# Kernel optimization log

Hardware: AMD Instinct MI355X
Metric: run time of the kernel (lower is better)

Reference implementation:

```python
import jax, jax.numpy as jnp
import numpy as np

N_HEADS = 16

def setup_inputs() -> dict:
    key = jax.random.key(0)
    ks = jax.random.split(key, 6)
    B, S, D = 2, 2048, 1024
    return {
        "hidden_states": jax.random.normal(ks[0], (B, S, D), dtype=jnp.float32),
        "Wq": jax.random.normal(ks[1], (D, D), dtype=jnp.float32) * (1.0 / np.sqrt(D)),
        "Wk": jax.random.normal(ks[2], (D, D), dtype=jnp.float32) * (1.0 / np.sqrt(D)),
        "Wv": jax.random.normal(ks[3], (D, D), dtype=jnp.float32) * (1.0 / np.sqrt(D)),
        "Wo": jax.random.normal(ks[4], (D, D), dtype=jnp.float32) * (1.0 / np.sqrt(D)),
        "bo": jnp.zeros((D,), dtype=jnp.float32),
    }

def reference(hidden_states, Wq, Wk, Wv, Wo, bo):
    B, S, D = hidden_states.shape
    H = N_HEADS
    hd = D // H  # head_dim; d_kv == d_model per module's final view
    # nn.Linear(bias=False): x @ W.T, then the module's direct view to (B, H, S, hd)
    q = (hidden_states @ Wq.T).reshape(B, H, S, hd)
    k = (hidden_states @ Wk.T).reshape(B, H, S, hd)  # self-attention path (encoder_states=None)
    v = (hidden_states @ Wv.T).reshape(B, H, S, hd)
    # naive full score matrix [B, H, S, S]
    wei = jnp.einsum('bhqd,bhkd->bhqk', q, k)
    causal = jnp.tril(jnp.ones((S, S), dtype=bool))
    wei = jnp.where(causal, wei, -jnp.inf)
    # NOTE: module divides logits by head_dim (not sqrt) -- preserved faithfully
    attn = jax.nn.softmax(wei / hd, axis=-1)
    ctx = jnp.einsum('bhqk,bhkd->bhqd', attn, v)  # [B, H, S, hd]
    out = ctx.transpose(0, 2, 1, 3).reshape(B, S, D)
    return out @ Wo.T + bo
```

## Files before the change

### kernel.cpp

```cpp
#include <hip/hip_runtime.h>

#define S_LEN   2048
#define D_MODEL 1024
#define N_HEADS 16
#define HEAD_DIM 64

typedef unsigned short u16;
typedef float  floatx4 __attribute__((ext_vector_type(4)));
typedef short  bf16x8  __attribute__((ext_vector_type(8)));
typedef short  bf16x4  __attribute__((ext_vector_type(4)));

__device__ __forceinline__ u16 f2bf(float f) {
    unsigned int u = __float_as_uint(f);
    u += 0x7FFF + ((u >> 16) & 1);
    return (u16)(u >> 16);
}
__device__ __forceinline__ unsigned pack2bf(float a, float b) {
    return (unsigned)f2bf(a) | ((unsigned)f2bf(b) << 16);
}

__device__ __forceinline__ void gload_lds16(const void* g, void* l) {
    __builtin_amdgcn_global_load_lds(
        reinterpret_cast<const __attribute__((address_space(1))) unsigned int*>(
            reinterpret_cast<uintptr_t>(g)),
        reinterpret_cast<__attribute__((address_space(3))) unsigned int*>(
            reinterpret_cast<uintptr_t>(l)),
        16, 0, 0);
}

__global__ __launch_bounds__(256) void cast_all(const float* __restrict__ hs,
                                                const float* __restrict__ w0,
                                                const float* __restrict__ w1,
                                                const float* __restrict__ w2,
                                                const float* __restrict__ w3,
                                                u16* __restrict__ dst) {
    const size_t NHS = (size_t)2 * S_LEN * D_MODEL;
    const size_t e0 = (size_t)blockIdx.x * 2048;
    const float* src;
    size_t base;
    if (e0 < NHS)                 { src = hs; base = 0; }
    else {
        const int wi = (int)((e0 - NHS) >> 20);
        src = wi == 0 ? w0 : wi == 1 ? w1 : wi == 2 ? w2 : w3;
        base = NHS + ((size_t)wi << 20);
    }
    const size_t i = e0 + (size_t)threadIdx.x * 8;
    const float4 a = *(const float4*)(src + (i - base));
    const float4 b = *(const float4*)(src + (i - base) + 4);
    uint4 o;
    o.x = pack2bf(a.x, a.y); o.y = pack2bf(a.z, a.w);
    o.z = pack2bf(b.x, b.y); o.w = pack2bf(b.z, b.w);
    *(uint4*)(dst + i) = o;
}

__global__ __launch_bounds__(256) void vtrans(const u16* __restrict__ Vf,
                                              u16* __restrict__ Vt) {
    __shared__ unsigned T[64 * 133];
    const int bh = blockIdx.y;
    const int sBase = blockIdx.x * 128;
    const u16* src = Vf + (size_t)bh * (S_LEN * HEAD_DIM) + (size_t)sBase * HEAD_DIM;
    u16* dst = Vt + (size_t)bh * (S_LEN * HEAD_DIM) + sBase;
    const int tid = threadIdx.x;

#pragma unroll
    for (int it = 0; it < 4; ++it) {
        const int idx = it * 256 + tid;
        const int row = idx >> 3, ch = idx & 7;
        const float4 v4 = *(const float4*)(src + row * 64 + ch * 8);
        const u16* vs = (const u16*)&v4;
#pragma unroll
        for (int j = 0; j < 8; ++j) T[(ch * 8 + j) * 133 + row] = vs[j];
    }
    __syncthreads();
#pragma unroll
    for (int it = 0; it < 4; ++it) {
        const int idx = it * 256 + tid;
        const int d = idx >> 4, sc = idx & 15;
        union { u16 u[8]; float4 f; } tmp;
#pragma unroll
        for (int j = 0; j < 8; ++j) tmp.u[j] = (u16)T[d * 133 + sc * 8 + j];
        *(float4*)(dst + (size_t)d * S_LEN + sc * 8) = tmp.f;
    }
}

__global__ __launch_bounds__(256, 3) void gemm_qkv(const u16* __restrict__ A,
                                                   const u16* __restrict__ Wq,
                                                   const u16* __restrict__ Wk,
                                                   const u16* __restrict__ Wv,
                                                   u16* __restrict__ Qo,
                                                   u16* __restrict__ Ko,
                                                   u16* __restrict__ Vfo) {
    __shared__ u16 As[128 * 64];
    __shared__ u16 Ws[128 * 64];

    const int blk = blockIdx.x;
    const int y   = (blk & 7) | (((blk >> 3) & 3) << 3);
    const int x   = blk >> 5;
    const int which = x >> 3;
    const int nBase = (x & 7) * 128;
    const int mBase = y * 128;
    const u16* W = which == 0 ? Wq : which == 1 ? Wk : Wv;

    const int tid = threadIdx.x, lane = tid & 63, wv = tid >> 6;
    const int l15 = lane & 15, quad = lane >> 4;
    const int wm = wv & 1, wn = wv >> 1;
    const int srow = lane >> 3;
    const int gch  = (lane & 7) ^ srow;
    const int swz  = l15 & 7;

    floatx4 acc[4][4];
#pragma unroll
    for (int i = 0; i < 4; ++i)
#pragma unroll
        for (int j = 0; j < 4; ++j) acc[i][j] = (floatx4)(0.0f);

    for (int k0 = 0; k0 < D_MODEL; k0 += 64) {
        __syncthreads();
#pragma unroll
        for (int t = 0; t < 4; ++t) {
            const int ci = wv * 4 + t;
            gload_lds16(A + (size_t)(mBase + ci * 8 + srow) * D_MODEL + k0 + gch * 8,
                        &As[ci * 512]);
            gload_lds16(W + (size_t)(nBase + ci * 8 + srow) * D_MODEL + k0 + gch * 8,
                        &Ws[ci * 512]);
        }
        __syncthreads();

#pragma unroll
        for (int ks = 0; ks < 2; ++ks) {
            bf16x8 af[4], bfr[4];
#pragma unroll
            for (int mt = 0; mt < 4; ++mt)
                af[mt] = *(const bf16x8*)&As[(wm * 64 + mt * 16 + l15) * 64
                                             + ((ks * 4 + quad) ^ swz) * 8];
#pragma unroll
            for (int nt = 0; nt < 4; ++nt)
                bfr[nt] = *(const bf16x8*)&Ws[(wn * 64 + nt * 16 + l15) * 64
                                              + ((ks * 4 + quad) ^ swz) * 8];
#pragma unroll
            for (int mt = 0; mt < 4; ++mt)
#pragma unroll
                for (int nt = 0; nt < 4; ++nt)
                    acc[mt][nt] = __builtin_amdgcn_mfma_f32_16x16x32_bf16(af[mt], bfr[nt], acc[mt][nt], 0, 0, 0);
        }
    }

    u16* O = which == 0 ? Qo : (which == 1 ? Ko : Vfo);
    const float scale = which == 0 ? (1.44269504088896f / 64.0f) : 1.0f;
#pragma unroll
    for (int mt = 0; mt < 4; ++mt)
#pragma unroll
        for (int nt = 0; nt < 4; ++nt) {
            const int col = nBase + wn * 64 + nt * 16 + l15;
#pragma unroll
            for (int r = 0; r < 4; ++r) {
                const int row = mBase + wm * 64 + mt * 16 + quad * 4 + r;
                O[(size_t)row * D_MODEL + col] = f2bf(acc[mt][nt][r] * scale);
            }
        }
}

__global__ __launch_bounds__(256, 3) void gemm_out(const u16* __restrict__ A,
                                                   const u16* __restrict__ W,
                                                   const float* __restrict__ bias,
                                                   float* __restrict__ C) {
    __shared__ u16 As[64 * 64];
    __shared__ u16 Ws[128 * 64];

    const int nBase = blockIdx.x * 128;
    const int mBase = blockIdx.y * 64;
    const int tid = threadIdx.x, lane = tid & 63, wv = tid >> 6;
    const int l15 = lane & 15, quad = lane >> 4;
    const int wm = wv & 1, wn = wv >> 1;
    const int srow = lane >> 3;
    const int gch  = (lane & 7) ^ srow;
    const int swz  = l15 & 7;

    floatx4 acc[2][4];
#pragma unroll
    for (int i = 0; i < 2; ++i)
#pragma unroll
        for (int j = 0; j < 4; ++j) acc[i][j] = (floatx4)(0.0f);

    for (int k0 = 0; k0 < D_MODEL; k0 += 64) {
        __syncthreads();
#pragma unroll
        for (int t = 0; t < 2; ++t) {
            const int ci = wv * 2 + t;
            gload_lds16(A + (size_t)(mBase + ci * 8 + srow) * D_MODEL + k0 + gch * 8,
                        &As[ci * 512]);
        }
#pragma unroll
        for (int t = 0; t < 4; ++t) {
            const int ci = wv * 4 + t;
            gload_lds16(W + (size_t)(nBase + ci * 8 + srow) * D_MODEL + k0 + gch * 8,
                        &Ws[ci * 512]);
        }
        __syncthreads();

#pragma unroll
        for (int ks = 0; ks < 2; ++ks) {
            bf16x8 af[2], bfr[4];
#pragma unroll
            for (int mt = 0; mt < 2; ++mt)
                af[mt] = *(const bf16x8*)&As[(wm * 32 + mt * 16 + l15) * 64
                                             + ((ks * 4 + quad) ^ swz) * 8];
#pragma unroll
            for (int nt = 0; nt < 4; ++nt)
                bfr[nt] = *(const bf16x8*)&Ws[(wn * 64 + nt * 16 + l15) * 64
                                              + ((ks * 4 + quad) ^ swz) * 8];
#pragma unroll
            for (int mt = 0; mt < 2; ++mt)
#pragma unroll
                for (int nt = 0; nt < 4; ++nt)
                    acc[mt][nt] = __builtin_amdgcn_mfma_f32_16x16x32_bf16(af[mt], bfr[nt], acc[mt][nt], 0, 0, 0);
        }
    }

#pragma unroll
    for (int mt = 0; mt < 2; ++mt)
#pragma unroll
        for (int nt = 0; nt < 4; ++nt) {
            const int col = nBase + wn * 64 + nt * 16 + l15;
            const float bv = bias[col];
#pragma unroll
            for (int r = 0; r < 4; ++r) {
                const int row = mBase + wm * 32 + mt * 16 + quad * 4 + r;
                C[(size_t)row * D_MODEL + col] = acc[mt][nt][r] + bv;
            }
        }
}

__global__ __launch_bounds__(256, 3) void attn6(const u16* __restrict__ Q,
                                                const u16* __restrict__ K,
                                                const u16* __restrict__ Vt,
                                                u16* __restrict__ Ctx) {
    __shared__ __align__(16) char smem[35840];
    u16*   Ks    = (u16*)smem;
    u16*   Vs    = (u16*)(smem + 16384);
    float* RedA  = (float*)smem;
    float* RedB  = (float*)(smem + 17408);
    float* lpbuf = (float*)(smem + 34816);

    const int flat = blockIdx.x;
    const int g    = flat & 31;
    const int qt   = 31 - (flat >> 5);
    const int h = g & 15, b = g >> 4;

    const int tid = threadIdx.x, lane = tid & 63, wv = tid >> 6;
    const int l15 = lane & 15, quad = lane >> 4;

    const size_t headOff = ((size_t)b * N_HEADS + h) * S_LEN * HEAD_DIM;
    const u16* Qh = Q + headOff;
    const u16* Kh = K + headOff;
    const u16* Vh = Vt + headOff;
    u16* Cb = Ctx + (size_t)b * S_LEN * D_MODEL + (size_t)h * HEAD_DIM;

    const int srow = lane >> 3;
    const int gch  = (lane & 7) ^ srow;
    const int swz  = l15 & 7;

    const int qBase = qt * 64;

    bf16x8 qb[4][2];
#pragma unroll
    for (int qg = 0; qg < 4; ++qg)
#pragma unroll
        for (int ks = 0; ks < 2; ++ks)
            qb[qg][ks] = *(const bf16x8*)(Qh + (size_t)(qBase + qg * 16 + l15) * 64
                                          + ks * 32 + quad * 8);

    floatx4 o[4][4];
#pragma unroll
    for (int qg = 0; qg < 4; ++qg)
#pragma unroll
        for (int dg = 0; dg < 4; ++dg) o[qg][dg] = (floatx4)(0.0f);
    float lp[4] = {0.0f, 0.0f, 0.0f, 0.0f};

#pragma unroll
    for (int t = 0; t < 2; ++t) {
        const int ci = wv * 2 + t;
        gload_lds16(Kh + (size_t)(ci * 8 + srow) * 64 + gch * 8, &Ks[ci * 512]);
        gload_lds16(Vh + (size_t)(ci * 8 + srow) * S_LEN + gch * 8, &Vs[ci * 512]);
    }
    __syncthreads();

    for (int kt = 0; kt <= qt; ++kt) {
        const int cur = (kt & 1) * 4096;
        const int nxt = 4096 - cur;

        if (kt < qt) {
            const int kB2 = (kt + 1) * 64;
#pragma unroll
            for (int t = 0; t < 2; ++t) {
                const int ci = wv * 2 + t;
                gload_lds16(Kh + (size_t)(kB2 + ci * 8 + srow) * 64 + gch * 8,
                            &Ks[nxt + ci * 512]);
                gload_lds16(Vh + (size_t)(ci * 8 + srow) * S_LEN + kB2 + gch * 8,
                            &Vs[nxt + ci * 512]);
            }
        }

        bf16x8 ka[2];
#pragma unroll
        for (int ks = 0; ks < 2; ++ks)
            ka[ks] = *(const bf16x8*)&Ks[cur + (wv * 16 + l15) * 64 + ((ks * 4 + quad) ^ swz) * 8];

        bf16x4 vb[4];
#pragma unroll
        for (int dg = 0; dg < 4; ++dg)
            vb[dg] = *(const bf16x4*)&Vs[cur + (dg * 16 + l15) * 64
                                         + (((wv * 2 + (quad >> 1)) ^ swz) * 8) + (quad & 1) * 4];

        floatx4 s[4];
#pragma unroll
        for (int qg = 0; qg < 4; ++qg) {
            s[qg] = (floatx4)(0.0f);
#pragma unroll
            for (int ks = 0; ks < 2; ++ks)
                s[qg] = __builtin_amdgcn_mfma_f32_16x16x32_bf16(ka[ks], qb[qg][ks], s[qg], 0, 0, 0);
        }

        const bool diag = (kt == qt);
#pragma unroll
        for (int qg = 0; qg < 4; ++qg) {
            if (diag && qg < wv) continue;
            float p[4];
#pragma unroll
            for (int r = 0; r < 4; ++r) {
                float pv = __builtin_amdgcn_exp2f(s[qg][r]);
                if (diag && qg == wv && (quad * 4 + r > l15)) pv = 0.0f;
                p[r] = pv;
                lp[qg] += pv;
            }
            union { uint2 u; bf16x4 v; } pk;
            pk.u.x = __builtin_amdgcn_perm(__float_as_uint(p[1]), __float_as_uint(p[0]), 0x07060302);
            pk.u.y = __builtin_amdgcn_perm(__float_as_uint(p[3]), __float_as_uint(p[2]), 0x07060302);
#pragma unroll
            for (int dg = 0; dg < 4; ++dg)
                o[qg][dg] = __builtin_amdgcn_mfma_f32_16x16x16bf16_1k(pk.v, vb[dg], o[qg][dg], 0, 0, 0);
        }

        __syncthreads();
    }

#pragma unroll
    for (int qg = 0; qg < 4; ++qg) {
        lp[qg] += __shfl_xor(lp[qg], 16);
        lp[qg] += __shfl_xor(lp[qg], 32);
    }
    lpbuf[wv * 64 + quad * 16 + l15] = lp[quad];

    if (wv == 1 || wv == 3) {
        float* R = (wv == 1) ? RedA : RedB;
#pragma unroll
        for (int qg = 0; qg < 4; ++qg)
#pragma unroll
            for (int dg = 0; dg < 4; ++dg)
                *(floatx4*)&R[(dg * 16 + l15) * 68 + qg * 16 + quad * 4] = o[qg][dg];
    }
    __syncthreads();
    if (wv == 0 || wv == 2) {
        const float* R = (wv == 0) ? RedA : RedB;
#pragma unroll
        for (int qg = 0; qg < 4; ++qg)
#pragma unroll
            for (int dg = 0; dg < 4; ++dg)
                o[qg][dg] += *(const floatx4*)&R[(dg * 16 + l15) * 68 + qg * 16 + quad * 4];
    }
    __syncthreads();
    if (wv == 2) {
#pragma unroll
        for (int qg = 0; qg < 4; ++qg)
#pragma unroll
            for (int dg = 0; dg < 4; ++dg)
                *(floatx4*)&RedA[(dg * 16 + l15) * 68 + qg * 16 + quad * 4] = o[qg][dg];
    }
    __syncthreads();
    if (wv == 0) {
#pragma unroll
        for (int qg = 0; qg < 4; ++qg) {
#pragma unroll
            for (int dg = 0; dg < 4; ++dg)
                o[qg][dg] += *(const floatx4*)&RedA[(dg * 16 + l15) * 68 + qg * 16 + quad * 4];
            floatx4 lt = *(const floatx4*)&lpbuf[0 * 64 + qg * 16 + quad * 4];
            lt += *(const floatx4*)&lpbuf[1 * 64 + qg * 16 + quad * 4];
            lt += *(const floatx4*)&lpbuf[2 * 64 + qg * 16 + quad * 4];
            lt += *(const floatx4*)&lpbuf[3 * 64 + qg * 16 + quad * 4];
#pragma unroll
            for (int r = 0; r < 4; ++r) {
                const float inv = 1.0f / lt[r];
                const int row = qBase + qg * 16 + quad * 4 + r;
#pragma unroll
                for (int dg = 0; dg < 4; ++dg)
                    Cb[(size_t)row * D_MODEL + dg * 16 + l15] = f2bf(o[qg][dg][r] * inv);
            }
        }
    }
}

extern "C" void kernel_launch(void* const* d_in, const int* in_sizes, int n_in,
                              void* d_out, int out_size, void* d_ws, size_t ws_size,
                              hipStream_t stream) {
    const float* hs = (const float*)d_in[0];
    const float* Wq = (const float*)d_in[1];
    const float* Wk = (const float*)d_in[2];
    const float* Wv = (const float*)d_in[3];
    const float* Wo = (const float*)d_in[4];
    const float* bo = (const float*)d_in[5];
    float* out = (float*)d_out;

    const size_t NHS = (size_t)2 * S_LEN * D_MODEL;
    const size_t NW  = (size_t)D_MODEL * D_MODEL;

    u16* hsb = (u16*)d_ws;
    u16* Wb  = hsb + NHS;
    u16* Qb  = Wb + 4 * NW;
    u16* Kb  = Qb + NHS;
    u16* Vfb = Kb + NHS;
    u16* Vtb = Vfb + NHS;
    u16* Cxb = Vtb + NHS;

    cast_all<<<4096, 256, 0, stream>>>(hs, Wq, Wk, Wv, Wo, hsb);

    gemm_qkv<<<768, 256, 0, stream>>>(hsb, Wb, Wb + NW, Wb + 2 * NW,
                                      Qb, Kb, Vfb);

    vtrans<<<dim3(16, 32), 256, 0, stream>>>(Vfb, Vtb);

    attn6<<<1024, 256, 0, stream>>>(Qb, Kb, Vtb, Cxb);

    gemm_out<<<dim3(8, 64), 256, 0, stream>>>(Cxb, Wb + 3 * NW, bo, out);
}
```

Measured before the change: 165.1 us.

## Drop V transpose kernel; read row-major V in attention with swapped MFMA operands

Removes the separate vtrans kernel and its extra global round trip. The attention kernel now loads V tiles in their natural row-major layout and gathers the B-operand with scalar u16 LDS reads. It swaps the PV MFMA operands so the output accumulators come out transposed, and reworks the cross-wave reduction and epilogue to match. It also raises wave priority around the MFMA section. The trade is one fewer launch and less memory traffic, against slower scalar LDS gathers in the inner loop and an extra reduction barrier.

```diff
diff --git a/kernel.cpp b/kernel.cpp
--- a/kernel.cpp
+++ b/kernel.cpp
@@ -53,36 +53,6 @@
     *(uint4*)(dst + i) = o;
 }
 
-__global__ __launch_bounds__(256) void vtrans(const u16* __restrict__ Vf,
-                                              u16* __restrict__ Vt) {
-    __shared__ unsigned T[64 * 133];
-    const int bh = blockIdx.y;
-    const int sBase = blockIdx.x * 128;
-    const u16* src = Vf + (size_t)bh * (S_LEN * HEAD_DIM) + (size_t)sBase * HEAD_DIM;
-    u16* dst = Vt + (size_t)bh * (S_LEN * HEAD_DIM) + sBase;
-    const int tid = threadIdx.x;
-
-#pragma unroll
-    for (int it = 0; it < 4; ++it) {
-        const int idx = it * 256 + tid;
-        const int row = idx >> 3, ch = idx & 7;
-        const float4 v4 = *(const float4*)(src + row * 64 + ch * 8);
-        const u16* vs = (const u16*)&v4;
-#pragma unroll
-        for (int j = 0; j < 8; ++j) T[(ch * 8 + j) * 133 + row] = vs[j];
-    }
-    __syncthreads();
-#pragma unroll
-    for (int it = 0; it < 4; ++it) {
-        const int idx = it * 256 + tid;
-        const int d = idx >> 4, sc = idx & 15;
-        union { u16 u[8]; float4 f; } tmp;
-#pragma unroll
-        for (int j = 0; j < 8; ++j) tmp.u[j] = (u16)T[d * 133 + sc * 8 + j];
-        *(float4*)(dst + (size_t)d * S_LEN + sc * 8) = tmp.f;
-    }
-}
-
 __global__ __launch_bounds__(256, 3) void gemm_qkv(const u16* __restrict__ A,
                                                    const u16* __restrict__ Wq,
                                                    const u16* __restrict__ Wk,
@@ -233,7 +203,7 @@
 
 __global__ __launch_bounds__(256, 3) void attn6(const u16* __restrict__ Q,
                                                 const u16* __restrict__ K,
-                                                const u16* __restrict__ Vt,
+                                                const u16* __restrict__ Vf,
                                                 u16* __restrict__ Ctx) {
     __shared__ __align__(16) char smem[35840];
     u16*   Ks    = (u16*)smem;
@@ -253,7 +223,7 @@
     const size_t headOff = ((size_t)b * N_HEADS + h) * S_LEN * HEAD_DIM;
     const u16* Qh = Q + headOff;
     const u16* Kh = K + headOff;
-    const u16* Vh = Vt + headOff;
+    const u16* Vh = Vf + headOff;
     u16* Cb = Ctx + (size_t)b * S_LEN * D_MODEL + (size_t)h * HEAD_DIM;
 
     const int srow = lane >> 3;
@@ -281,7 +251,7 @@
     for (int t = 0; t < 2; ++t) {
         const int ci = wv * 2 + t;
         gload_lds16(Kh + (size_t)(ci * 8 + srow) * 64 + gch * 8, &Ks[ci * 512]);
-        gload_lds16(Vh + (size_t)(ci * 8 + srow) * S_LEN + gch * 8, &Vs[ci * 512]);
+        gload_lds16(Vh + (size_t)(ci * 8 + srow) * 64 + gch * 8, &Vs[ci * 512]);
     }
     __syncthreads();
 
@@ -296,7 +266,7 @@
                 const int ci = wv * 2 + t;
                 gload_lds16(Kh + (size_t)(kB2 + ci * 8 + srow) * 64 + gch * 8,
                             &Ks[nxt + ci * 512]);
-                gload_lds16(Vh + (size_t)(ci * 8 + srow) * S_LEN + kB2 + gch * 8,
+                gload_lds16(Vh + (size_t)(kB2 + ci * 8 + srow) * 64 + gch * 8,
                             &Vs[nxt + ci * 512]);
             }
         }
@@ -308,10 +278,21 @@
 
         bf16x4 vb[4];
 #pragma unroll
-        for (int dg = 0; dg < 4; ++dg)
-            vb[dg] = *(const bf16x4*)&Vs[cur + (dg * 16 + l15) * 64
-                                         + (((wv * 2 + (quad >> 1)) ^ swz) * 8) + (quad & 1) * 4];
-
+        for (int dg = 0; dg < 4; ++dg) {
+            u16 tmp[4];
+#pragma unroll
+            for (int j = 0; j < 4; ++j) {
+                const int R = wv * 16 + quad * 4 + j;
+                const int d = dg * 16 + l15;
+                const int slot = (d >> 3) ^ (R & 7);
+                tmp[j] = Vs[cur + R * 64 + slot * 8 + (d & 7)];
+            }
+            bf16x4 v; v[0] = (short)tmp[0]; v[1] = (short)tmp[1];
+            v[2] = (short)tmp[2]; v[3] = (short)tmp[3];
+            vb[dg] = v;
+        }
+
+        __builtin_amdgcn_s_setprio(1);
         floatx4 s[4];
 #pragma unroll
         for (int qg = 0; qg < 4; ++qg) {
@@ -338,8 +319,9 @@
             pk.u.y = __builtin_amdgcn_perm(__float_as_uint(p[3]), __float_as_uint(p[2]), 0x07060302);
 #pragma unroll
             for (int dg = 0; dg < 4; ++dg)
-                o[qg][dg] = __builtin_amdgcn_mfma_f32_16x16x16bf16_1k(pk.v, vb[dg], o[qg][dg], 0, 0, 0);
-        }
+                o[qg][dg] = __builtin_amdgcn_mfma_f32_16x16x16bf16_1k(vb[dg], pk.v, o[qg][dg], 0, 0, 0);
+        }
+        __builtin_amdgcn_s_setprio(0);
 
         __syncthreads();
     }
@@ -357,7 +339,9 @@
         for (int qg = 0; qg < 4; ++qg)
 #pragma unroll
             for (int dg = 0; dg < 4; ++dg)
-                *(floatx4*)&R[(dg * 16 + l15) * 68 + qg * 16 + quad * 4] = o[qg][dg];
+#pragma unroll
+                for (int r = 0; r < 4; ++r)
+                    R[(dg * 16 + quad * 4 + r) * 68 + qg * 16 + l15] = o[qg][dg][r];
     }
     __syncthreads();
     if (wv == 0 || wv == 2) {
@@ -366,7 +350,9 @@
         for (int qg = 0; qg < 4; ++qg)
 #pragma unroll
             for (int dg = 0; dg < 4; ++dg)
-                o[qg][dg] += *(const floatx4*)&R[(dg * 16 + l15) * 68 + qg * 16 + quad * 4];
+#pragma unroll
+                for (int r = 0; r < 4; ++r)
+                    o[qg][dg][r] += R[(dg * 16 + quad * 4 + r) * 68 + qg * 16 + l15];
     }
     __syncthreads();
     if (wv == 2) {
@@ -374,15 +360,27 @@
         for (int qg = 0; qg < 4; ++qg)
 #pragma unroll
             for (int dg = 0; dg < 4; ++dg)
-                *(floatx4*)&RedA[(dg * 16 + l15) * 68 + qg * 16 + quad * 4] = o[qg][dg];
+#pragma unroll
+                for (int r = 0; r < 4; ++r)
+                    RedA[(dg * 16 + quad * 4 + r) * 68 + qg * 16 + l15] = o[qg][dg][r];
     }
     __syncthreads();
     if (wv == 0) {
 #pragma unroll
+        for (int qg = 0; qg < 4; ++qg)
+#pragma unroll
+            for (int dg = 0; dg < 4; ++dg)
+#pragma unroll
+                for (int r = 0; r < 4; ++r) {
+                    const float v = o[qg][dg][r]
+                        + RedA[(dg * 16 + quad * 4 + r) * 68 + qg * 16 + l15];
+                    RedB[(dg * 16 + quad * 4 + r) * 68 + qg * 16 + l15] = v;
+                }
+    }
+    __syncthreads();
+    if (wv == 0) {
+#pragma unroll
         for (int qg = 0; qg < 4; ++qg) {
-#pragma unroll
-            for (int dg = 0; dg < 4; ++dg)
-                o[qg][dg] += *(const floatx4*)&RedA[(dg * 16 + l15) * 68 + qg * 16 + quad * 4];
             floatx4 lt = *(const floatx4*)&lpbuf[0 * 64 + qg * 16 + quad * 4];
             lt += *(const floatx4*)&lpbuf[1 * 64 + qg * 16 + quad * 4];
             lt += *(const floatx4*)&lpbuf[2 * 64 + qg * 16 + quad * 4];
@@ -392,8 +390,10 @@
                 const float inv = 1.0f / lt[r];
                 const int row = qBase + qg * 16 + quad * 4 + r;
 #pragma unroll
-                for (int dg = 0; dg < 4; ++dg)
-                    Cb[(size_t)row * D_MODEL + dg * 16 + l15] = f2bf(o[qg][dg][r] * inv);
+                for (int dg = 0; dg < 4; ++dg) {
+                    const float v = RedB[(dg * 16 + l15) * 68 + qg * 16 + quad * 4 + r];
+                    Cb[(size_t)row * D_MODEL + dg * 16 + l15] = f2bf(v * inv);
+                }
             }
         }
     }
@@ -418,17 +418,14 @@
     u16* Qb  = Wb + 4 * NW;
     u16* Kb  = Qb + NHS;
     u16* Vfb = Kb + NHS;
-    u16* Vtb = Vfb + NHS;
-    u16* Cxb = Vtb + NHS;
+    u16* Cxb = Vfb + NHS;
 
     cast_all<<<4096, 256, 0, stream>>>(hs, Wq, Wk, Wv, Wo, hsb);
 
     gemm_qkv<<<768, 256, 0, stream>>>(hsb, Wb, Wb + NW, Wb + 2 * NW,
                                       Qb, Kb, Vfb);
 
-    vtrans<<<dim3(16, 32), 256, 0, stream>>>(Vfb, Vtb);
-
-    attn6<<<1024, 256, 0, stream>>>(Qb, Kb, Vtb, Cxb);
+    attn6<<<1024, 256, 0, stream>>>(Qb, Kb, Vfb, Cxb);
 
     gemm_out<<<dim3(8, 64), 256, 0, stream>>>(Cxb, Wb + 3 * NW, bo, out);
 }
```

Result: no change. 166.9 us (+1.1%).

## Merge two adjacent query tiles per 512-thread attention block sharing K/V tiles

Applied to the files above, without the earlier changes.

The attention kernel now runs 8 waves per block, with two 64-row query tiles (paired as 2qp and 2qp+1) sharing each staged K/V tile. This halves global-to-LDS K/V traffic per query row and halves the block count. The block order is also changed so heavy and light causal pairs interleave for better load balance. The cost is more LDS per block (about 70 KB) and idle waves on the lower tile's final key step. It also needs a larger reduction scratch area.

```diff
diff --git a/kernel.cpp b/kernel.cpp
--- a/kernel.cpp
+++ b/kernel.cpp
@@ -231,24 +231,27 @@
         }
 }
 
-__global__ __launch_bounds__(256, 3) void attn6(const u16* __restrict__ Q,
+__global__ __launch_bounds__(512, 4) void attn8(const u16* __restrict__ Q,
                                                 const u16* __restrict__ K,
                                                 const u16* __restrict__ Vt,
                                                 u16* __restrict__ Ctx) {
-    __shared__ __align__(16) char smem[35840];
+    __shared__ __align__(16) char smem[71680];
     u16*   Ks    = (u16*)smem;
     u16*   Vs    = (u16*)(smem + 16384);
-    float* RedA  = (float*)smem;
-    float* RedB  = (float*)(smem + 17408);
-    float* lpbuf = (float*)(smem + 34816);
+    float* lpbuf = (float*)(smem + 69632);
 
     const int flat = blockIdx.x;
     const int g    = flat & 31;
-    const int qt   = 31 - (flat >> 5);
+    const int jj   = flat >> 5;
+    const int qp   = (jj < 8) ? (15 - jj) : (jj - 8);
     const int h = g & 15, b = g >> 4;
 
     const int tid = threadIdx.x, lane = tid & 63, wv = tid >> 6;
+    const int kw = wv & 3, qh = wv >> 2;
     const int l15 = lane & 15, quad = lane >> 4;
+
+    float* R0 = (float*)(smem + qh * 34816);
+    float* R1 = (float*)(smem + qh * 34816 + 17408);
 
     const size_t headOff = ((size_t)b * N_HEADS + h) * S_LEN * HEAD_DIM;
     const u16* Qh = Q + headOff;
@@ -260,7 +263,9 @@
     const int gch  = (lane & 7) ^ srow;
     const int swz  = l15 & 7;
 
-    const int qBase = qt * 64;
+    const int qBase = (qp * 2 + qh) * 64;
+    const int qtw   = qp * 2 + qh;
+    const int qtmax = qp * 2 + 1;
 
     bf16x8 qb[4][2];
 #pragma unroll
@@ -277,68 +282,63 @@
         for (int dg = 0; dg < 4; ++dg) o[qg][dg] = (floatx4)(0.0f);
     float lp[4] = {0.0f, 0.0f, 0.0f, 0.0f};
 
-#pragma unroll
-    for (int t = 0; t < 2; ++t) {
-        const int ci = wv * 2 + t;
-        gload_lds16(Kh + (size_t)(ci * 8 + srow) * 64 + gch * 8, &Ks[ci * 512]);
-        gload_lds16(Vh + (size_t)(ci * 8 + srow) * S_LEN + gch * 8, &Vs[ci * 512]);
-    }
+    gload_lds16(Kh + (size_t)(wv * 8 + srow) * 64 + gch * 8, &Ks[wv * 512]);
+    gload_lds16(Vh + (size_t)(wv * 8 + srow) * S_LEN + gch * 8, &Vs[wv * 512]);
     __syncthreads();
 
-    for (int kt = 0; kt <= qt; ++kt) {
+    for (int kt = 0; kt <= qtmax; ++kt) {
         const int cur = (kt & 1) * 4096;
         const int nxt = 4096 - cur;
 
-        if (kt < qt) {
+        if (kt < qtmax) {
             const int kB2 = (kt + 1) * 64;
-#pragma unroll
-            for (int t = 0; t < 2; ++t) {
-                const int ci = wv * 2 + t;
-                gload_lds16(Kh + (size_t)(kB2 + ci * 8 + srow) * 64 + gch * 8,
-                            &Ks[nxt + ci * 512]);
-                gload_lds16(Vh + (size_t)(ci * 8 + srow) * S_LEN + kB2 + gch * 8,
-                            &Vs[nxt + ci * 512]);
+            gload_lds16(Kh + (size_t)(kB2 + wv * 8 + srow) * 64 + gch * 8,
+                        &Ks[nxt + wv * 512]);
+            gload_lds16(Vh + (size_t)(wv * 8 + srow) * S_LEN + kB2 + gch * 8,
+                        &Vs[nxt + wv * 512]);
+        }
+
+        if (kt <= qtw) {
+            bf16x8 ka[2];
+#pragma unroll
+            for (int ks = 0; ks < 2; ++ks)
+                ka[ks] = *(const bf16x8*)&Ks[cur + (kw * 16 + l15) * 64
+                                             + ((ks * 4 + quad) ^ swz) * 8];
+
+            bf16x4 vb[4];
+#pragma unroll
+            for (int dg = 0; dg < 4; ++dg)
+                vb[dg] = *(const bf16x4*)&Vs[cur + (dg * 16 + l15) * 64
+                                             + (((kw * 2 + (quad >> 1)) ^ swz) * 8) + (quad & 1) * 4];
+
+            floatx4 s[4];
+#pragma unroll
+            for (int qg = 0; qg < 4; ++qg) {
+                s[qg] = (floatx4)(0.0f);
+#pragma unroll
+                for (int ks = 0; ks < 2; ++ks)
+                    s[qg] = __builtin_amdgcn_mfma_f32_16x16x32_bf16(ka[ks], qb[qg][ks], s[qg], 0, 0, 0);
             }
-        }
-
-        bf16x8 ka[2];
-#pragma unroll
-        for (int ks = 0; ks < 2; ++ks)
-            ka[ks] = *(const bf16x8*)&Ks[cur + (wv * 16 + l15) * 64 + ((ks * 4 + quad) ^ swz) * 8];
-
-        bf16x4 vb[4];
-#pragma unroll
-        for (int dg = 0; dg < 4; ++dg)
-            vb[dg] = *(const bf16x4*)&Vs[cur + (dg * 16 + l15) * 64
-                                         + (((wv * 2 + (quad >> 1)) ^ swz) * 8) + (quad & 1) * 4];
-
-        floatx4 s[4];
-#pragma unroll
-        for (int qg = 0; qg < 4; ++qg) {
-            s[qg] = (floatx4)(0.0f);
-#pragma unroll
-            for (int ks = 0; ks < 2; ++ks)
-                s[qg] = __builtin_amdgcn_mfma_f32_16x16x32_bf16(ka[ks], qb[qg][ks], s[qg], 0, 0, 0);
-        }
-
-        const bool diag = (kt == qt);
-#pragma unroll
-        for (int qg = 0; qg < 4; ++qg) {
-            if (diag && qg < wv) continue;
-            float p[4];
-#pragma unroll
-            for (int r = 0; r < 4; ++r) {
-                float pv = __builtin_amdgcn_exp2f(s[qg][r]);
-                if (diag && qg == wv && (quad * 4 + r > l15)) pv = 0.0f;
-                p[r] = pv;
-                lp[qg] += pv;
+
+            const bool diag = (kt == qtw);
+#pragma unroll
+            for (int qg = 0; qg < 4; ++qg) {
+                if (diag && qg < kw) continue;
+                float p[4];
+#pragma unroll
+                for (int r = 0; r < 4; ++r) {
+                    float pv = __builtin_amdgcn_exp2f(s[qg][r]);
+                    if (diag && qg == kw && (quad * 4 + r > l15)) pv = 0.0f;
+                    p[r] = pv;
+                    lp[qg] += pv;
+                }
+                union { uint2 u; bf16x4 v; } pk;
+                pk.u.x = __builtin_amdgcn_perm(__float_as_uint(p[1]), __float_as_uint(p[0]), 0x07060302);
+                pk.u.y = __builtin_amdgcn_perm(__float_as_uint(p[3]), __float_as_uint(p[2]), 0x07060302);
+#pragma unroll
+                for (int dg = 0; dg < 4; ++dg)
+                    o[qg][dg] = __builtin_amdgcn_mfma_f32_16x16x16bf16_1k(pk.v, vb[dg], o[qg][dg], 0, 0, 0);
             }
-            union { uint2 u; bf16x4 v; } pk;
-            pk.u.x = __builtin_amdgcn_perm(__float_as_uint(p[1]), __float_as_uint(p[0]), 0x07060302);
-            pk.u.y = __builtin_amdgcn_perm(__float_as_uint(p[3]), __float_as_uint(p[2]), 0x07060302);
-#pragma unroll
-            for (int dg = 0; dg < 4; ++dg)
-                o[qg][dg] = __builtin_amdgcn_mfma_f32_16x16x16bf16_1k(pk.v, vb[dg], o[qg][dg], 0, 0, 0);
         }
 
         __syncthreads();
@@ -349,10 +349,10 @@
         lp[qg] += __shfl_xor(lp[qg], 16);
         lp[qg] += __shfl_xor(lp[qg], 32);
     }
-    lpbuf[wv * 64 + quad * 16 + l15] = lp[quad];
-
-    if (wv == 1 || wv == 3) {
-        float* R = (wv == 1) ? RedA : RedB;
+    lpbuf[qh * 256 + kw * 64 + quad * 16 + l15] = lp[quad];
+
+    if (kw == 1 || kw == 3) {
+        float* R = (kw == 1) ? R0 : R1;
 #pragma unroll
         for (int qg = 0; qg < 4; ++qg)
 #pragma unroll
@@ -360,8 +360,8 @@
                 *(floatx4*)&R[(dg * 16 + l15) * 68 + qg * 16 + quad * 4] = o[qg][dg];
     }
     __syncthreads();
-    if (wv == 0 || wv == 2) {
-        const float* R = (wv == 0) ? RedA : RedB;
+    if (kw == 0 || kw == 2) {
+        const float* R = (kw == 0) ? R0 : R1;
 #pragma unroll
         for (int qg = 0; qg < 4; ++qg)
 #pragma unroll
@@ -369,24 +369,24 @@
                 o[qg][dg] += *(const floatx4*)&R[(dg * 16 + l15) * 68 + qg * 16 + quad * 4];
     }
     __syncthreads();
-    if (wv == 2) {
+    if (kw == 2) {
 #pragma unroll
         for (int qg = 0; qg < 4; ++qg)
 #pragma unroll
             for (int dg = 0; dg < 4; ++dg)
-                *(floatx4*)&RedA[(dg * 16 + l15) * 68 + qg * 16 + quad * 4] = o[qg][dg];
+                *(floatx4*)&R0[(dg * 16 + l15) * 68 + qg * 16 + quad * 4] = o[qg][dg];
     }
     __syncthreads();
-    if (wv == 0) {
+    if (kw == 0) {
 #pragma unroll
         for (int qg = 0; qg < 4; ++qg) {
 #pragma unroll
             for (int dg = 0; dg < 4; ++dg)
-                o[qg][dg] += *(const floatx4*)&RedA[(dg * 16 + l15) * 68 + qg * 16 + quad * 4];
-            floatx4 lt = *(const floatx4*)&lpbuf[0 * 64 + qg * 16 + quad * 4];
-            lt += *(const floatx4*)&lpbuf[1 * 64 + qg * 16 + quad * 4];
-            lt += *(const floatx4*)&lpbuf[2 * 64 + qg * 16 + quad * 4];
-            lt += *(const floatx4*)&lpbuf[3 * 64 + qg * 16 + quad * 4];
+                o[qg][dg] += *(const floatx4*)&R0[(dg * 16 + l15) * 68 + qg * 16 + quad * 4];
+            floatx4 lt = *(const floatx4*)&lpbuf[qh * 256 + 0 * 64 + qg * 16 + quad * 4];
+            lt += *(const floatx4*)&lpbuf[qh * 256 + 1 * 64 + qg * 16 + quad * 4];
+            lt += *(const floatx4*)&lpbuf[qh * 256 + 2 * 64 + qg * 16 + quad * 4];
+            lt += *(const floatx4*)&lpbuf[qh * 256 + 3 * 64 + qg * 16 + quad * 4];
 #pragma unroll
             for (int r = 0; r < 4; ++r) {
                 const float inv = 1.0f / lt[r];
@@ -428,7 +428,7 @@
 
     vtrans<<<dim3(16, 32), 256, 0, stream>>>(Vfb, Vtb);
 
-    attn6<<<1024, 256, 0, stream>>>(Qb, Kb, Vtb, Cxb);
+    attn8<<<512, 512, 0, stream>>>(Qb, Kb, Vtb, Cxb);
 
     gemm_out<<<dim3(8, 64), 256, 0, stream>>>(Cxb, Wb + 3 * NW, bo, out);
 }
```

Measured after the change: 218.6 us. +32.4%, slower.
